# Performance work log

Hardware: AMD Instinct MI355X
Metric: run time of the kernel (lower is better)

## Reference

```python
import jax, jax.numpy as jnp
import numpy as np

L, B, T, D, H, F = 6, 4, 1024, 512, 8, 2048
DH = D // H
BIAS_DIM = 2
E = 65536
EPS = 1e-3  # LayerNormalization default epsilon in the source


def _ln(x, scale, bias):
    m = jnp.mean(x, axis=-1, keepdims=True)
    v = jnp.mean(jnp.square(x - m), axis=-1, keepdims=True)  # tf.nn.moments: population variance
    return (x - m) * jax.lax.rsqrt(v + EPS) * scale + bias


def setup_inputs() -> dict:
    key = jax.random.key(0)
    ks = jax.random.split(key, 24)
    g = lambda k, shape: (jax.random.normal(k, shape, jnp.float32) * (shape[-1] ** -0.5))
    states = jax.random.normal(ks[0], (B, T, D), jnp.float32)
    # causal mask broadcast over heads: [B, 1, Tq, Tk]
    masks = jnp.tril(jnp.ones((T, T), jnp.float32))[None, None] * jnp.ones((B, 1, 1, 1), jnp.float32)
    # sparse bias edges: columns (edge_type, batch_idx, key_idx, query_idx)
    et = jax.random.randint(ks[1], (E, 1), 0, BIAS_DIM)
    bi = jax.random.randint(ks[2], (E, 1), 0, B)
    ki = jax.random.randint(ks[3], (E, 1), 0, T)
    qi = jax.random.randint(ks[4], (E, 1), 0, T)
    attention_bias = jnp.concatenate([et, bi, ki, qi], axis=1).astype(jnp.int32)
    return dict(
        states=states,
        masks=masks,
        attention_bias=attention_bias,
        Wq=g(ks[5], (L, D, H, DH)),
        Wk=g(ks[6], (L, D, H, DH)),
        Wv=g(ks[7], (L, D, H, DH)),
        Wo=g(ks[8], (L, H, DH, D)),
        Eb=g(ks[9], (L, BIAS_DIM, DH)),
        Es=g(ks[10], (L, DH)),
        ln1_s=jnp.ones((L, D), jnp.float32),
        ln1_b=jnp.zeros((L, D), jnp.float32),
        ln2_s=jnp.ones((L, D), jnp.float32),
        ln2_b=jnp.zeros((L, D), jnp.float32),
        lno_s=jnp.ones((D,), jnp.float32),
        lno_b=jnp.zeros((D,), jnp.float32),
        W1=g(ks[11], (L, D, F)),
        b1=jnp.zeros((L, F), jnp.float32),
        W2=g(ks[12], (L, F, D)),
        b2=jnp.zeros((L, D), jnp.float32),
    )


def reference(states, masks, attention_bias, Wq, Wk, Wv, Wo, Eb, Es,
              ln1_s, ln1_b, ln2_s, ln2_b, lno_s, lno_b, W1, b1, W2, b2):
    FMIN = jnp.finfo(jnp.float32).min
    scale = jnp.float32(DH) ** -0.5
    et, bi, ki, qi = (attention_bias[:, 0], attention_bias[:, 1],
                      attention_bias[:, 2], attention_bias[:, 3])
    for l in range(L):
        # --- self-attention with edge bias ---
        x = _ln(states, ln1_s[l], ln1_b[l])
        q = jnp.einsum('btd,dha->btha', x, Wq[l])
        k = jnp.einsum('btd,dha->btha', x, Wk[l])
        v = jnp.einsum('btd,dha->btha', x, Wv[l])
        alpha = jnp.einsum('bkha,bqha->bhqk', k, q)
        # edge-type embedding -> scalar per edge, scatter into dense [B,q,k] (duplicates sum)
        bias_val = Eb[l][et] @ Es[l]  # [E]
        bias3 = jnp.zeros((B, T, T), jnp.float32).at[bi, ki, qi].add(bias_val)
        alpha = alpha + jnp.einsum('bqk,bkh->bhqk', bias3, k.sum(-1))
        alpha = alpha * scale
        alpha = alpha * masks + (1.0 - jnp.ceil(masks)) * FMIN
        alpha = jax.nn.softmax(alpha, axis=-1) * masks  # mask-softmax-renormalize (no renorm, just re-mask)
        ctx = jnp.einsum('bhqk,bkha->bqha', alpha, v)
        states = states + jnp.einsum('btha,had->btd', ctx, Wo[l])
        # --- FFN ---
        h = jax.nn.relu(_ln(states, ln2_s[l], ln2_b[l]) @ W1[l] + b1[l])
        states = states + h @ W2[l] + b2[l]
    return _ln(states, lno_s, lno_b)
```

## Files before the change

kernel.cpp:

```cpp
#include <hip/hip_runtime.h>
#include <hip/hip_bf16.h>
#include <cstdint>

#define LNUM 6
#define BNUM 4
#define TSEQ 1024
#define DMOD 512
#define HNUM 8
#define FDIM 2048
#define DHEAD 64
#define NEVENTS 65536
#define EPS_LN 1e-3f
#define ATT_SCALE 0.125f

#define GF_ACC 1
#define GF_RELU 2
#define GF_BIAS 4
#define GF_SPLIT 8
#define GF_QKV 16
#define GF_PART 32

typedef float f32x4 __attribute__((ext_vector_type(4)));
typedef short bf16x8 __attribute__((ext_vector_type(8)));
typedef unsigned short u16;
typedef unsigned int u32;

__device__ inline u16 f2bf(float f){
  u32 u = __builtin_bit_cast(u32, f);
  u32 r = (u + 0x7fffu + ((u >> 16) & 1u)) >> 16;
  return (u16)r;
}
__device__ inline float bf2f(u16 u){
  return __builtin_bit_cast(float, (u32)u << 16);
}
__device__ inline void split2(float x, u16 &hi, u16 &lo){
  u16 h = f2bf(x);
  lo = f2bf(x - bf2f(h));
  hi = h;
}
__device__ inline void gload16(const void* g, void* l){
  __builtin_amdgcn_global_load_lds(
      (const __attribute__((address_space(1))) void*)g,
      (__attribute__((address_space(3))) void*)l, 16, 0, 0);
}

__global__ __launch_bounds__(256) void ln_kernel(const float* __restrict__ x,
    const float* __restrict__ s, const float* __restrict__ bsh,
    float* __restrict__ yf, u16* __restrict__ yh, u16* __restrict__ yl, int mode){
  int row = blockIdx.x, tid = threadIdx.x;
  const float* xr = x + (size_t)row * DMOD;
  float2 v = *reinterpret_cast<const float2*>(xr + tid*2);
  float sum = v.x + v.y, sq = v.x*v.x + v.y*v.y;
  #pragma unroll
  for (int off = 32; off > 0; off >>= 1){
    sum += __shfl_down(sum, off);
    sq  += __shfl_down(sq, off);
  }
  __shared__ float ss[4], sq2[4];
  int wid = tid >> 6;
  if ((tid & 63) == 0){ ss[wid] = sum; sq2[wid] = sq; }
  __syncthreads();
  sum = ss[0]+ss[1]+ss[2]+ss[3];
  sq  = sq2[0]+sq2[1]+sq2[2]+sq2[3];
  float mean = sum * (1.f/DMOD);
  float var  = sq * (1.f/DMOD) - mean*mean;
  float rstd = rsqrtf(var + EPS_LN);
  float2 sc = *reinterpret_cast<const float2*>(s + tid*2);
  float2 bi = *reinterpret_cast<const float2*>(bsh + tid*2);
  float ox = (v.x - mean)*rstd*sc.x + bi.x;
  float oy = (v.y - mean)*rstd*sc.y + bi.y;
  if (mode == 0){
    u16 h0,l0,h1,l1;
    split2(ox,h0,l0); split2(oy,h1,l1);
    *(u32*)(yh + (size_t)row*DMOD + tid*2) = (u32)h0 | ((u32)h1<<16);
    *(u32*)(yl + (size_t)row*DMOD + tid*2) = (u32)l0 | ((u32)l1<<16);
  } else {
    float2 o; o.x = ox; o.y = oy;
    *reinterpret_cast<float2*>(yf + (size_t)row*DMOD + tid*2) = o;
  }
}

__global__ __launch_bounds__(256) void wsplit5(
    const float* __restrict__ Wq, const float* __restrict__ Wk,
    const float* __restrict__ Wv, const float* __restrict__ Wo,
    const float* __restrict__ W1, int l,
    u16* __restrict__ wqkvh, u16* __restrict__ wqkvl,
    u16* __restrict__ woh,   u16* __restrict__ wol,
    u16* __restrict__ w1h,   u16* __restrict__ w1l){
  __shared__ float T[64][65];
  int id = blockIdx.x;
  const float* src; u16 *dh, *dl; int N, bx, by;
  if (id < 256){
    const int which = id >> 6, sub = id & 63;
    bx = sub & 7; by = sub >> 3; N = 512;
    if (which == 0){ src = Wq; dh = wqkvh;            dl = wqkvl; }
    else if (which == 1){ src = Wk; dh = wqkvh + 512*512; dl = wqkvl + 512*512; }
    else if (which == 2){ src = Wv; dh = wqkvh + 2*512*512; dl = wqkvl + 2*512*512; }
    else { src = Wo; dh = woh; dl = wol; }
    src += (size_t)l*DMOD*DMOD;
  } else {
    id -= 256;
    bx = id & 31; by = id >> 5; N = 2048;
    src = W1 + (size_t)l*DMOD*FDIM; dh = w1h; dl = w1l;
  }
  const int k0 = by*64, n0 = bx*64;
  const int tid = threadIdx.x;
  {
    const int r = tid>>2, cseg = (tid&3)*16;
    const float* sp = src + (size_t)(k0+r)*N + n0 + cseg;
    #pragma unroll
    for (int i = 0; i < 16; i += 4){
      float4 v = *(const float4*)(sp + i);
      T[cseg+i+0][r] = v.x; T[cseg+i+1][r] = v.y;
      T[cseg+i+2][r] = v.z; T[cseg+i+3][r] = v.w;
    }
  }
  __syncthreads();
  const int n = tid>>2, kseg = (tid&3)*16;
  u32 wh[8], wl[8];
  #pragma unroll
  for (int i = 0; i < 8; ++i){
    u16 h0,l0,h1,l1;
    split2(T[n][kseg+2*i], h0, l0);
    split2(T[n][kseg+2*i+1], h1, l1);
    wh[i] = (u32)h0 | ((u32)h1<<16);
    wl[i] = (u32)l0 | ((u32)l1<<16);
  }
  u16* ph = dh + (size_t)(n0+n)*DMOD + k0 + kseg;
  u16* pl = dl + (size_t)(n0+n)*DMOD + k0 + kseg;
  *(uint4*)(ph)   = make_uint4(wh[0],wh[1],wh[2],wh[3]);
  *(uint4*)(ph+8) = make_uint4(wh[4],wh[5],wh[6],wh[7]);
  *(uint4*)(pl)   = make_uint4(wl[0],wl[1],wl[2],wl[3]);
  *(uint4*)(pl+8) = make_uint4(wl[4],wl[5],wl[6],wl[7]);
}

__global__ __launch_bounds__(256) void wsplit(const float* __restrict__ W,
    u16* __restrict__ Thi, u16* __restrict__ Tlo, int K, int N){
  __shared__ float T[64][65];
  const int k0 = blockIdx.y*64, n0 = blockIdx.x*64;
  const int tid = threadIdx.x;
  {
    const int r = tid>>2, cseg = (tid&3)*16;
    const float* src = W + (size_t)(k0+r)*N + n0 + cseg;
    #pragma unroll
    for (int i = 0; i < 16; i += 4){
      float4 v = *(const float4*)(src + i);
      T[cseg+i+0][r] = v.x; T[cseg+i+1][r] = v.y;
      T[cseg+i+2][r] = v.z; T[cseg+i+3][r] = v.w;
    }
  }
  __syncthreads();
  const int n = tid>>2, kseg = (tid&3)*16;
  u32 wh[8], wl[8];
  #pragma unroll
  for (int i = 0; i < 8; ++i){
    u16 h0,l0,h1,l1;
    split2(T[n][kseg+2*i], h0, l0);
    split2(T[n][kseg+2*i+1], h1, l1);
    wh[i] = (u32)h0 | ((u32)h1<<16);
    wl[i] = (u32)l0 | ((u32)l1<<16);
  }
  u16* dh = Thi + (size_t)(n0+n)*K + k0 + kseg;
  u16* dl = Tlo + (size_t)(n0+n)*K + k0 + kseg;
  *(uint4*)(dh)   = make_uint4(wh[0],wh[1],wh[2],wh[3]);
  *(uint4*)(dh+8) = make_uint4(wh[4],wh[5],wh[6],wh[7]);
  *(uint4*)(dl)   = make_uint4(wl[0],wl[1],wl[2],wl[3]);
  *(uint4*)(dl+8) = make_uint4(wl[4],wl[5],wl[6],wl[7]);
}

template<int BN, int NS, int FLAGS>
__global__ __launch_bounds__(256) void gemm_mfma(
    const u16* __restrict__ Ahi, const u16* __restrict__ Alo,
    const u16* __restrict__ Bhi, const u16* __restrict__ Blo,
    const float* __restrict__ bias, float* __restrict__ C,
    u16* __restrict__ Ohi, u16* __restrict__ Olo,
    u16* __restrict__ Vhi, u16* __restrict__ Vlo,
    int M, int N, int K, int kc){
  constexpr int NA  = 16;
  constexpr int NB  = BN/8;
  constexpr int PER = (NA+NB)/4;
  __shared__ __align__(16) unsigned char As[128*128];
  __shared__ __align__(16) unsigned char Bs[BN*128];
  const int tid = threadIdx.x, wid = tid>>6, lane = tid&63;
  const int li = lane&15, g = lane>>4;
  const int nxb = N/BN;
  const int cpx = gridDim.x >> 3;
  const int bid = blockIdx.x;
  const int wg  = (bid&7)*cpx + (bid>>3);
  const int bx = wg % nxb, by = wg / nxb;
  const int m0 = by*128, n0 = bx*BN;
  const int wr = wid>>1, wc = wid&1;
  const int kbeg = blockIdx.y * kc, kend = kbeg + kc;
  f32x4 acc[4][NS] = {};

  for (int k0 = kbeg; k0 < kend; k0 += 32){
    __syncthreads();
    #pragma unroll
    for (int i = 0; i < PER; ++i){
      const int issue = wid*PER + i;
      const bool isA = issue < NA;
      const int ia = isA ? issue : issue - NA;
      const int c = ia*64 + lane;
      const int row = c>>3, slot = c&7;
      const int sg = slot ^ (row&7);
      const u16* base = isA ? (sg < 4 ? Ahi : Alo) : (sg < 4 ? Bhi : Blo);
      const int gr = (isA ? m0 : n0) + row;
      const u16* gp = base + (size_t)gr*K + k0 + (sg&3)*8;
      unsigned char* lp = (isA ? As : Bs) + ia*1024 + lane*16;
      gload16(gp, lp);
    }
    __syncthreads();
    bf16x8 ah[4], al[4], bh[NS], bl[NS];
    #pragma unroll
    for (int ms = 0; ms < 4; ++ms){
      const int r = wr*64 + ms*16 + li; const int x = (r&7)<<4;
      const unsigned char* p = As + r*128;
      ah[ms] = *(const bf16x8*)(p + ((g*16)^x));
      al[ms] = *(const bf16x8*)(p + ((64 + g*16)^x));
    }
    #pragma unroll
    for (int ns = 0; ns < NS; ++ns){
      const int r = wc*(BN/2) + ns*16 + li; const int x = (r&7)<<4;
      const unsigned char* p = Bs + r*128;
      bh[ns] = *(const bf16x8*)(p + ((g*16)^x));
      bl[ns] = *(const bf16x8*)(p + ((64 + g*16)^x));
    }
    #pragma unroll
    for (int ms = 0; ms < 4; ++ms)
      #pragma unroll
      for (int ns = 0; ns < NS; ++ns){
        acc[ms][ns] = __builtin_amdgcn_mfma_f32_16x16x32_bf16(ah[ms], bh[ns], acc[ms][ns], 0, 0, 0);
        acc[ms][ns] = __builtin_amdgcn_mfma_f32_16x16x32_bf16(ah[ms], bl[ns], acc[ms][ns], 0, 0, 0);
        acc[ms][ns] = __builtin_amdgcn_mfma_f32_16x16x32_bf16(al[ms], bh[ns], acc[ms][ns], 0, 0, 0);
      }
  }
  #pragma unroll
  for (int ms = 0; ms < 4; ++ms){
    #pragma unroll
    for (int ns = 0; ns < NS; ++ns){
      #pragma unroll
      for (int r = 0; r < 4; ++r){
        const int m = m0 + wr*64 + ms*16 + g*4 + r;
        const int n = n0 + wc*(BN/2) + ns*16 + li;
        float val = acc[ms][ns][r];
        if (FLAGS & GF_BIAS) val += bias[n];
        if (FLAGS & GF_RELU) val = fmaxf(val, 0.f);
        if (FLAGS & GF_QKV){
          u16 vh, vl; split2(val, vh, vl);
          if (n < 1024){
            const size_t ix = (size_t)m*1024 + n;
            Ohi[ix] = vh; Olo[ix] = vl;
          } else {
            const size_t ix = ((size_t)(m>>10)*DMOD + (n-1024))*TSEQ + (m&1023);
            Vhi[ix] = vh; Vlo[ix] = vl;
          }
        } else if (FLAGS & GF_SPLIT){
          u16 vh, vl; split2(val, vh, vl);
          const size_t ix = (size_t)m*N + n;
          Ohi[ix] = vh; Olo[ix] = vl;
        } else if (FLAGS & GF_PART){
          C[(size_t)blockIdx.y*M*N + (size_t)m*N + n] = val;
        } else {
          const size_t ix = (size_t)m*N + n;
          if (FLAGS & GF_ACC) val += C[ix];
          C[ix] = val;
        }
      }
    }
  }
}

__global__ __launch_bounds__(256) void red2(const float* __restrict__ part,
    const float* __restrict__ bias, float* __restrict__ states, int hasb){
  const size_t MN = (size_t)BNUM*TSEQ*DMOD;
  const size_t i4 = ((size_t)blockIdx.x*256 + threadIdx.x)*4;
  float4 a = *(const float4*)(part + i4);
  float4 b = *(const float4*)(part + MN + i4);
  float4 s = *(const float4*)(states + i4);
  s.x += a.x + b.x;
  s.y += a.y + b.y;
  s.z += a.z + b.z;
  s.w += a.w + b.w;
  if (hasb){
    float4 bb = *(const float4*)(bias + (int)(i4 & (DMOD-1)));
    s.x += bb.x; s.y += bb.y; s.z += bb.z; s.w += bb.w;
  }
  *(float4*)(states + i4) = s;
}

__global__ __launch_bounds__(256) void ksum_kernel(const u16* __restrict__ kh_,
    const u16* __restrict__ kl_, float* __restrict__ ks){
  int idx = blockIdx.x*256 + threadIdx.x;
  const size_t base = (size_t)(idx>>3)*1024 + 512 + (idx&7)*DHEAD;
  const u16* ph = kh_ + base;
  const u16* pl = kl_ + base;
  float s = 0.f;
  #pragma unroll
  for (int a = 0; a < DHEAD; a += 8){
    bf16x8 vh = *(const bf16x8*)(ph + a);
    bf16x8 vl = *(const bf16x8*)(pl + a);
    #pragma unroll
    for (int j = 0; j < 8; ++j) s += bf2f((u16)vh[j]) + bf2f((u16)vl[j]);
  }
  ks[idx] = s;
}

__global__ __launch_bounds__(256) void scatter_kernel(const int* __restrict__ ab,
    const float* __restrict__ Eb, const float* __restrict__ Es, float* __restrict__ bias3){
  __shared__ float d2[2];
  if (threadIdx.x < 2){
    float v = 0.f;
    #pragma unroll
    for (int a = 0; a < DHEAD; ++a) v += Eb[threadIdx.x*DHEAD + a]*Es[a];
    d2[threadIdx.x] = v;
  }
  __syncthreads();
  int e = blockIdx.x*256 + threadIdx.x;
  int4 r = *reinterpret_cast<const int4*>(ab + (size_t)e*4);
  atomicAdd(bias3 + ((size_t)r.y*TSEQ + r.z)*TSEQ + r.w, d2[r.x]);
}

__device__ __forceinline__ void tile_compute(
    const unsigned char* __restrict__ Klh, const unsigned char* __restrict__ Kll,
    const unsigned char* __restrict__ Vh, const unsigned char* __restrict__ Vl,
    unsigned char* __restrict__ Plh, unsigned char* __restrict__ Pll,
    const float* __restrict__ ksl, const float* __restrict__ bb,
    int kt, int rowg0, int wid, int li, int g,
    const bf16x8* qah, const bf16x8* qal,
    f32x4* oacc, float* mrun, float* srun){
  f32x4 sacc[4] = {};
  #pragma unroll
  for (int jb = 0; jb < 4; ++jb){
    const int rb = (jb*16 + li)*128, x = (li & 7) << 4;
    #pragma unroll
    for (int k2 = 0; k2 < 2; ++k2){
      bf16x8 kfh = *(const bf16x8*)(Klh + rb + ((g*16 + k2*64)^x));
      bf16x8 kfl = *(const bf16x8*)(Kll + rb + ((g*16 + k2*64)^x));
      sacc[jb] = __builtin_amdgcn_mfma_f32_16x16x32_bf16(qah[k2], kfh, sacc[jb], 0, 0, 0);
      sacc[jb] = __builtin_amdgcn_mfma_f32_16x16x32_bf16(qah[k2], kfl, sacc[jb], 0, 0, 0);
      sacc[jb] = __builtin_amdgcn_mfma_f32_16x16x32_bf16(qal[k2], kfh, sacc[jb], 0, 0, 0);
    }
  }
  #pragma unroll
  for (int jb = 0; jb < 4; ++jb){
    const int colg = kt + jb*16 + li;
    const float ksv = ksl[jb*16 + li];
    #pragma unroll
    for (int r = 0; r < 4; ++r){
      const int rowg = rowg0 + r;
      float s = (sacc[jb][r] + bb[(size_t)rowg*TSEQ + colg] * ksv) * ATT_SCALE;
      sacc[jb][r] = (colg <= rowg) ? s : -INFINITY;
    }
  }
  #pragma unroll
  for (int r = 0; r < 4; ++r){
    float tm = fmaxf(fmaxf(sacc[0][r], sacc[1][r]), fmaxf(sacc[2][r], sacc[3][r]));
    tm = fmaxf(tm, __shfl_xor(tm, 1));
    tm = fmaxf(tm, __shfl_xor(tm, 2));
    tm = fmaxf(tm, __shfl_xor(tm, 4));
    tm = fmaxf(tm, __shfl_xor(tm, 8));
    const float nm = fmaxf(mrun[r], tm);
    const float fac = __expf(mrun[r] - nm);
    mrun[r] = nm;
    float p0 = __expf(sacc[0][r] - nm);
    float p1 = __expf(sacc[1][r] - nm);
    float p2 = __expf(sacc[2][r] - nm);
    float p3 = __expf(sacc[3][r] - nm);
    float rs = p0 + p1 + p2 + p3;
    rs += __shfl_xor(rs, 1);
    rs += __shfl_xor(rs, 2);
    rs += __shfl_xor(rs, 4);
    rs += __shfl_xor(rs, 8);
    srun[r] = srun[r]*fac + rs;
    oacc[0][r] *= fac; oacc[1][r] *= fac; oacc[2][r] *= fac; oacc[3][r] *= fac;
    const int prow = g*4 + r;
    const int pb = wid*2048 + prow*128, px = (prow & 7) << 4;
    u16 ph0,pl0, ph1,pl1, ph2,pl2, ph3,pl3;
    split2(p0,ph0,pl0); split2(p1,ph1,pl1); split2(p2,ph2,pl2); split2(p3,ph3,pl3);
    *(u16*)(Plh + pb + ((li*2 +  0)^px)) = ph0;
    *(u16*)(Plh + pb + ((li*2 + 32)^px)) = ph1;
    *(u16*)(Plh + pb + ((li*2 + 64)^px)) = ph2;
    *(u16*)(Plh + pb + ((li*2 + 96)^px)) = ph3;
    *(u16*)(Pll + pb + ((li*2 +  0)^px)) = pl0;
    *(u16*)(Pll + pb + ((li*2 + 32)^px)) = pl1;
    *(u16*)(Pll + pb + ((li*2 + 64)^px)) = pl2;
    *(u16*)(Pll + pb + ((li*2 + 96)^px)) = pl3;
  }
  bf16x8 pah[2], pal[2];
  {
    const int pb = wid*2048 + li*128, x = (li & 7) << 4;
    pah[0] = *(const bf16x8*)(Plh + pb + ((g*16     )^x));
    pah[1] = *(const bf16x8*)(Plh + pb + ((g*16 + 64)^x));
    pal[0] = *(const bf16x8*)(Pll + pb + ((g*16     )^x));
    pal[1] = *(const bf16x8*)(Pll + pb + ((g*16 + 64)^x));
  }
  #pragma unroll
  for (int ja = 0; ja < 4; ++ja){
    const int vb = (ja*16 + li)*128, x = (li & 7) << 4;
    #pragma unroll
    for (int k2 = 0; k2 < 2; ++k2){
      bf16x8 vfh = *(const bf16x8*)(Vh + vb + ((g*16 + k2*64)^x));
      bf16x8 vfl = *(const bf16x8*)(Vl + vb + ((g*16 + k2*64)^x));
      oacc[ja] = __builtin_amdgcn_mfma_f32_16x16x32_bf16(pah[k2], vfh, oacc[ja], 0, 0, 0);
      oacc[ja] = __builtin_amdgcn_mfma_f32_16x16x32_bf16(pah[k2], vfl, oacc[ja], 0, 0, 0);
      oacc[ja] = __builtin_amdgcn_mfma_f32_16x16x32_bf16(pal[k2], vfh, oacc[ja], 0, 0, 0);
    }
  }
}

__global__ __launch_bounds__(256) void attn_split(
    const u16* __restrict__ qkh, const u16* __restrict__ qkl,
    const u16* __restrict__ vth, const u16* __restrict__ vtl,
    const float* __restrict__ ksum, const float* __restrict__ bias3,
    u16* __restrict__ ch_, u16* __restrict__ cl_){
  __shared__ __align__(16) unsigned char Klh[8192], Kll[8192], Vh[8192], Vl[8192];
  __shared__ __align__(16) unsigned char Plh[8192], Pll[8192];
  __shared__ float ksl[64];

  const int bid = blockIdx.x;
  const int p = bid & 7, h = (bid >> 3) & 7, b = bid >> 6;
  const int qA0 = p*64, qB0 = (15-p)*64;
  const int tid = threadIdx.x, wid = tid >> 6, lane = tid & 63;
  const int li = lane & 15, g = lane >> 4;
  const int rowA0 = qA0 + wid*16 + g*4;
  const int rowB0 = qB0 + wid*16 + g*4;

  bf16x8 qahA[2], qalA[2], qahB[2], qalB[2];
  {
    const size_t offA = (size_t)(b*TSEQ + qA0 + wid*16 + li)*1024 + h*DHEAD;
    const size_t offB = (size_t)(b*TSEQ + qB0 + wid*16 + li)*1024 + h*DHEAD;
    #pragma unroll
    for (int k2 = 0; k2 < 2; ++k2){
      qahA[k2] = *(const bf16x8*)(qkh + offA + g*8 + k2*32);
      qalA[k2] = *(const bf16x8*)(qkl + offA + g*8 + k2*32);
      qahB[k2] = *(const bf16x8*)(qkh + offB + g*8 + k2*32);
      qalB[k2] = *(const bf16x8*)(qkl + offB + g*8 + k2*32);
    }
  }

  f32x4 oaccA[4] = {}, oaccB[4] = {};
  float mrunA[4] = {-INFINITY,-INFINITY,-INFINITY,-INFINITY};
  float mrunB[4] = {-INFINITY,-INFINITY,-INFINITY,-INFINITY};
  float srunA[4] = {0.f,0.f,0.f,0.f};
  float srunB[4] = {0.f,0.f,0.f,0.f};

  const int krow = tid >> 2, part = tid & 3;
  const int lbase = krow*128, lx = (krow & 7) << 4;
  const float* bb = bias3 + (size_t)b*TSEQ*TSEQ;

  uint4 rk0, rk1, rk2, rk3, rv0, rv1, rv2, rv3;
  float ksr = 0.f;
  auto issue = [&](int kt){
    const size_t koff = (size_t)(b*TSEQ + kt + krow)*1024 + 512 + h*DHEAD + part*16;
    rk0 = *(const uint4*)(qkh + koff);
    rk1 = *(const uint4*)(qkh + koff + 8);
    rk2 = *(const uint4*)(qkl + koff);
    rk3 = *(const uint4*)(qkl + koff + 8);
    const size_t voff = ((size_t)b*DMOD + h*DHEAD + krow)*TSEQ + kt + part*16;
    rv0 = *(const uint4*)(vth + voff);
    rv1 = *(const uint4*)(vth + voff + 8);
    rv2 = *(const uint4*)(vtl + voff);
    rv3 = *(const uint4*)(vtl + voff + 8);
    if (tid < 64) ksr = ksum[(size_t)(b*TSEQ + kt + tid)*HNUM + h];
  };

  issue(0);
  for (int kt = 0; kt <= qB0; kt += 64){
    *(uint4*)(Klh + lbase + ((part*32     )^lx)) = rk0;
    *(uint4*)(Klh + lbase + ((part*32 + 16)^lx)) = rk1;
    *(uint4*)(Kll + lbase + ((part*32     )^lx)) = rk2;
    *(uint4*)(Kll + lbase + ((part*32 + 16)^lx)) = rk3;
    *(uint4*)(Vh  + lbase + ((part*32     )^lx)) = rv0;
    *(uint4*)(Vh  + lbase + ((part*32 + 16)^lx)) = rv1;
    *(uint4*)(Vl  + lbase + ((part*32     )^lx)) = rv2;
    *(uint4*)(Vl  + lbase + ((part*32 + 16)^lx)) = rv3;
    if (tid < 64) ksl[tid] = ksr;
    __syncthreads();
    if (kt + 64 <= qB0) issue(kt + 64);
    tile_compute(Klh, Kll, Vh, Vl, Plh, Pll, ksl, bb, kt, rowB0, wid, li, g,
                 qahB, qalB, oaccB, mrunB, srunB);
    if (kt <= qA0)
      tile_compute(Klh, Kll, Vh, Vl, Plh, Pll, ksl, bb, kt, rowA0, wid, li, g,
                   qahA, qalA, oaccA, mrunA, srunA);
    __syncthreads();
  }

  #pragma unroll
  for (int ja = 0; ja < 4; ++ja){
    #pragma unroll
    for (int r = 0; r < 4; ++r){
      {
        const float val = oaccB[ja][r] / srunB[r];
        u16 vh, vl; split2(val, vh, vl);
        const size_t ix = (size_t)(b*TSEQ + rowB0 + r)*DMOD + h*DHEAD + ja*16 + li;
        ch_[ix] = vh; cl_[ix] = vl;
      }
      {
        const float val = oaccA[ja][r] / srunA[r];
        u16 vh, vl; split2(val, vh, vl);
        const size_t ix = (size_t)(b*TSEQ + rowA0 + r)*DMOD + h*DHEAD + ja*16 + li;
        ch_[ix] = vh; cl_[ix] = vl;
      }
    }
  }
}

extern "C" void kernel_launch(void* const* d_in, const int* in_sizes, int n_in,
                              void* d_out, int out_size, void* d_ws, size_t ws_size,
                              hipStream_t stream){
  const float* states0 = (const float*)d_in[0];
  const int*   ab      = (const int*)d_in[2];
  const float* Wq = (const float*)d_in[3];
  const float* Wk = (const float*)d_in[4];
  const float* Wv = (const float*)d_in[5];
  const float* Wo = (const float*)d_in[6];
  const float* Eb = (const float*)d_in[7];
  const float* Es = (const float*)d_in[8];
  const float* ln1_s = (const float*)d_in[9];
  const float* ln1_b = (const float*)d_in[10];
  const float* ln2_s = (const float*)d_in[11];
  const float* ln2_b = (const float*)d_in[12];
  const float* lno_s = (const float*)d_in[13];
  const float* lno_b = (const float*)d_in[14];
  const float* W1 = (const float*)d_in[15];
  const float* b1 = (const float*)d_in[16];
  const float* W2 = (const float*)d_in[17];
  const float* b2 = (const float*)d_in[18];
  float* out = (float*)d_out;

  char* ws = (char*)d_ws;
  const size_t MB = 1024*1024;
  float* states = (float*)(ws);
  u16* xh  = (u16*)(ws + 8*MB);
  u16* xl  = (u16*)(ws + 12*MB);
  u16* qkh = (u16*)(ws + 16*MB);
  u16* qkl = (u16*)(ws + 24*MB);
  u16* vth = (u16*)(ws + 32*MB);
  u16* vtl = (u16*)(ws + 36*MB);
  u16* cth = (u16*)(ws + 40*MB);
  u16* ctl = (u16*)(ws + 44*MB);
  float* ksum  = (float*)(ws + 48*MB);
  float* bias3 = (float*)(ws + 48*MB + 131072);
  char*  wA    = ws + 64*MB + 131072;
  char*  wB    = wA + 4*MB;
  u16* hh = qkh;
  u16* hl = vth;
  float* part = bias3;

  u16* wqkvh = (u16*)(wA);
  u16* wqkvl = (u16*)(wA + 1536*1024);
  u16* woh   = (u16*)(wA + 3*MB);
  u16* wol   = (u16*)(wA + 3*MB + 512*1024);
  u16* w2h   = (u16*)(wA);
  u16* w2l   = (u16*)(wA + 2*MB);
  u16* w1h   = (u16*)(wB);
  u16* w1l   = (u16*)(wB + 2*MB);

  hipMemcpyAsync(states, states0, 8*MB, hipMemcpyDeviceToDevice, stream);

  const int NROW = BNUM*TSEQ;
  dim3 blk(256);
  for (int l = 0; l < LNUM; ++l){
    wsplit5<<<512, blk, 0, stream>>>(Wq, Wk, Wv, Wo, W1, l,
        wqkvh, wqkvl, woh, wol, w1h, w1l);

    ln_kernel<<<NROW, blk, 0, stream>>>(states, ln1_s + l*DMOD, ln1_b + l*DMOD, nullptr, xh, xl, 0);
    gemm_mfma<128,4, GF_SPLIT|GF_QKV><<<384, blk, 0, stream>>>(
        xh, xl, wqkvh, wqkvl, nullptr, nullptr, qkh, qkl, vth, vtl, NROW, 1536, DMOD, DMOD);
    ksum_kernel<<<(BNUM*TSEQ*HNUM)/256, blk, 0, stream>>>(qkh, qkl, ksum);
    hipMemsetAsync(bias3, 0, (size_t)BNUM*TSEQ*TSEQ*sizeof(float), stream);
    scatter_kernel<<<NEVENTS/256, blk, 0, stream>>>(ab, Eb + (size_t)l*2*DHEAD, Es + (size_t)l*DHEAD, bias3);
    attn_split<<<BNUM*HNUM*8, blk, 0, stream>>>(qkh, qkl, vth, vtl, ksum, bias3, cth, ctl);
    gemm_mfma<64,2, GF_PART><<<dim3(256,2), blk, 0, stream>>>(
        cth, ctl, woh, wol, nullptr, part, nullptr, nullptr, nullptr, nullptr, NROW, DMOD, DMOD, DMOD/2);
    red2<<<(NROW*DMOD)/1024, blk, 0, stream>>>(part, b2, states, 0);

    wsplit<<<dim3(8,32), blk, 0, stream>>>(W2 + (size_t)l*FDIM*DMOD, w2h, w2l, FDIM, DMOD);
    ln_kernel<<<NROW, blk, 0, stream>>>(states, ln2_s + l*DMOD, ln2_b + l*DMOD, nullptr, xh, xl, 0);
    gemm_mfma<128,4, GF_BIAS|GF_RELU|GF_SPLIT><<<512, blk, 0, stream>>>(
        xh, xl, w1h, w1l, b1 + (size_t)l*FDIM, nullptr, hh, hl, nullptr, nullptr, NROW, FDIM, DMOD, DMOD);
    gemm_mfma<64,2, GF_PART><<<dim3(256,2), blk, 0, stream>>>(
        hh, hl, w2h, w2l, nullptr, part, nullptr, nullptr, nullptr, nullptr, NROW, DMOD, FDIM, FDIM/2);
    red2<<<(NROW*DMOD)/1024, blk, 0, stream>>>(part, b2 + (size_t)l*DMOD, states, 1);
  }
  ln_kernel<<<NROW, blk, 0, stream>>>(states, lno_s, lno_b, out, nullptr, nullptr, 1);
}
```

Baseline: 1.314 ms.

## Fuse split-K reduction into layernorm and split attention KV loop across two groups

The red2 reduction kernels are removed. Summing the two split-K partials plus the FFN bias into the residual now happens inside the following layernorm kernel, which writes the updated states back. Attention blocks grow to 512 threads: two 256-thread groups process alternating key tiles with separate LDS buffers, then merge their online-softmax states (max, sum, output) through shared memory. This cuts one launch and one full read/write pass per residual add, and doubles per-block parallelism over the key loop, at the cost of about 97KB of LDS per block and an extra merge step.

```diff
diff --git a/kernel.cpp b/kernel.cpp
--- a/kernel.cpp
+++ b/kernel.cpp
@@ -44,12 +44,24 @@
       (__attribute__((address_space(3))) void*)l, 16, 0, 0);
 }
 
-__global__ __launch_bounds__(256) void ln_kernel(const float* __restrict__ x,
+__global__ __launch_bounds__(256) void ln_kernel(float* __restrict__ x,
+    const float* __restrict__ part, const float* __restrict__ abias,
     const float* __restrict__ s, const float* __restrict__ bsh,
     float* __restrict__ yf, u16* __restrict__ yh, u16* __restrict__ yl, int mode){
   int row = blockIdx.x, tid = threadIdx.x;
-  const float* xr = x + (size_t)row * DMOD;
+  float* xr = x + (size_t)row * DMOD;
   float2 v = *reinterpret_cast<const float2*>(xr + tid*2);
+  if (part){
+    const size_t MN = (size_t)BNUM*TSEQ*DMOD;
+    const size_t o = (size_t)row*DMOD + tid*2;
+    float2 p0 = *reinterpret_cast<const float2*>(part + o);
+    float2 p1 = *reinterpret_cast<const float2*>(part + MN + o);
+    v.x += p0.x + p1.x; v.y += p0.y + p1.y;
+    if (abias){
+      v.x += abias[tid*2]; v.y += abias[tid*2+1];
+    }
+    *reinterpret_cast<float2*>(xr + tid*2) = v;
+  }
   float sum = v.x + v.y, sq = v.x*v.x + v.y*v.y;
   #pragma unroll
   for (int off = 32; off > 0; off >>= 1){
@@ -268,24 +280,6 @@
       }
     }
   }
-}
-
-__global__ __launch_bounds__(256) void red2(const float* __restrict__ part,
-    const float* __restrict__ bias, float* __restrict__ states, int hasb){
-  const size_t MN = (size_t)BNUM*TSEQ*DMOD;
-  const size_t i4 = ((size_t)blockIdx.x*256 + threadIdx.x)*4;
-  float4 a = *(const float4*)(part + i4);
-  float4 b = *(const float4*)(part + MN + i4);
-  float4 s = *(const float4*)(states + i4);
-  s.x += a.x + b.x;
-  s.y += a.y + b.y;
-  s.z += a.z + b.z;
-  s.w += a.w + b.w;
-  if (hasb){
-    float4 bb = *(const float4*)(bias + (int)(i4 & (DMOD-1)));
-    s.x += bb.x; s.y += bb.y; s.z += bb.z; s.w += bb.w;
-  }
-  *(float4*)(states + i4) = s;
 }
 
 __global__ __launch_bounds__(256) void ksum_kernel(const u16* __restrict__ kh_,
@@ -408,27 +402,39 @@
   }
 }
 
-__global__ __launch_bounds__(256) void attn_split(
+__global__ __launch_bounds__(512) void attn_split(
     const u16* __restrict__ qkh, const u16* __restrict__ qkl,
     const u16* __restrict__ vth, const u16* __restrict__ vtl,
     const float* __restrict__ ksum, const float* __restrict__ bias3,
     u16* __restrict__ ch_, u16* __restrict__ cl_){
-  __shared__ __align__(16) unsigned char Klh[8192], Kll[8192], Vh[8192], Vl[8192];
-  __shared__ __align__(16) unsigned char Plh[8192], Pll[8192];
-  __shared__ float ksl[64];
+  __shared__ __align__(16) unsigned char smem[99328];
+  unsigned char* PlhAll = smem + 65536;
+  unsigned char* PllAll = smem + 81920;
+  float* kslAll = (float*)(smem + 98304);
 
   const int bid = blockIdx.x;
   const int p = bid & 7, h = (bid >> 3) & 7, b = bid >> 6;
   const int qA0 = p*64, qB0 = (15-p)*64;
-  const int tid = threadIdx.x, wid = tid >> 6, lane = tid & 63;
-  const int li = lane & 15, g = lane >> 4;
-  const int rowA0 = qA0 + wid*16 + g*4;
-  const int rowB0 = qB0 + wid*16 + g*4;
+  const int tid = threadIdx.x;
+  const int grp = tid >> 8, t = tid & 255;
+  const int wid = tid >> 6;
+  const int wid4 = t >> 6;
+  const int lane = tid & 63, li = lane & 15, g = lane >> 4;
+  const int rowA0 = qA0 + wid4*16 + g*4;
+  const int rowB0 = qB0 + wid4*16 + g*4;
+  const int NB = 16 - p, NA = p + 1;
+  const int ITER = (NB + 1) >> 1;
+
+  unsigned char* Klh = smem + grp*32768;
+  unsigned char* Kll = Klh + 8192;
+  unsigned char* Vh  = Klh + 16384;
+  unsigned char* Vl  = Klh + 24576;
+  float* kslg = kslAll + grp*64;
 
   bf16x8 qahA[2], qalA[2], qahB[2], qalB[2];
   {
-    const size_t offA = (size_t)(b*TSEQ + qA0 + wid*16 + li)*1024 + h*DHEAD;
-    const size_t offB = (size_t)(b*TSEQ + qB0 + wid*16 + li)*1024 + h*DHEAD;
+    const size_t offA = (size_t)(b*TSEQ + qA0 + wid4*16 + li)*1024 + h*DHEAD;
+    const size_t offB = (size_t)(b*TSEQ + qB0 + wid4*16 + li)*1024 + h*DHEAD;
     #pragma unroll
     for (int k2 = 0; k2 < 2; ++k2){
       qahA[k2] = *(const bf16x8*)(qkh + offA + g*8 + k2*32);
@@ -444,7 +450,7 @@
   float srunA[4] = {0.f,0.f,0.f,0.f};
   float srunB[4] = {0.f,0.f,0.f,0.f};
 
-  const int krow = tid >> 2, part = tid & 3;
+  const int krow = t >> 2, part = t & 3;
   const int lbase = krow*128, lx = (krow & 7) << 4;
   const float* bb = bias3 + (size_t)b*TSEQ*TSEQ;
 
@@ -461,45 +467,90 @@
     rv1 = *(const uint4*)(vth + voff + 8);
     rv2 = *(const uint4*)(vtl + voff);
     rv3 = *(const uint4*)(vtl + voff + 8);
-    if (tid < 64) ksr = ksum[(size_t)(b*TSEQ + kt + tid)*HNUM + h];
+    if (t < 64) ksr = ksum[(size_t)(b*TSEQ + kt + t)*HNUM + h];
   };
 
-  issue(0);
-  for (int kt = 0; kt <= qB0; kt += 64){
-    *(uint4*)(Klh + lbase + ((part*32     )^lx)) = rk0;
-    *(uint4*)(Klh + lbase + ((part*32 + 16)^lx)) = rk1;
-    *(uint4*)(Kll + lbase + ((part*32     )^lx)) = rk2;
-    *(uint4*)(Kll + lbase + ((part*32 + 16)^lx)) = rk3;
-    *(uint4*)(Vh  + lbase + ((part*32     )^lx)) = rv0;
-    *(uint4*)(Vh  + lbase + ((part*32 + 16)^lx)) = rv1;
-    *(uint4*)(Vl  + lbase + ((part*32     )^lx)) = rv2;
-    *(uint4*)(Vl  + lbase + ((part*32 + 16)^lx)) = rv3;
-    if (tid < 64) ksl[tid] = ksr;
+  issue(grp*64);
+  for (int it = 0; it < ITER; ++it){
+    const int idx = it*2 + grp;
+    const bool act = idx < NB;
+    if (act){
+      *(uint4*)(Klh + lbase + ((part*32     )^lx)) = rk0;
+      *(uint4*)(Klh + lbase + ((part*32 + 16)^lx)) = rk1;
+      *(uint4*)(Kll + lbase + ((part*32     )^lx)) = rk2;
+      *(uint4*)(Kll + lbase + ((part*32 + 16)^lx)) = rk3;
+      *(uint4*)(Vh  + lbase + ((part*32     )^lx)) = rv0;
+      *(uint4*)(Vh  + lbase + ((part*32 + 16)^lx)) = rv1;
+      *(uint4*)(Vl  + lbase + ((part*32     )^lx)) = rv2;
+      *(uint4*)(Vl  + lbase + ((part*32 + 16)^lx)) = rv3;
+      if (t < 64) kslg[t] = ksr;
+    }
     __syncthreads();
-    if (kt + 64 <= qB0) issue(kt + 64);
-    tile_compute(Klh, Kll, Vh, Vl, Plh, Pll, ksl, bb, kt, rowB0, wid, li, g,
-                 qahB, qalB, oaccB, mrunB, srunB);
-    if (kt <= qA0)
-      tile_compute(Klh, Kll, Vh, Vl, Plh, Pll, ksl, bb, kt, rowA0, wid, li, g,
-                   qahA, qalA, oaccA, mrunA, srunA);
+    if (idx + 2 < NB) issue((idx + 2)*64);
+    if (act){
+      const int kt = idx*64;
+      tile_compute(Klh, Kll, Vh, Vl, PlhAll, PllAll, kslg, bb, kt, rowB0,
+                   wid, li, g, qahB, qalB, oaccB, mrunB, srunB);
+      if (idx < NA)
+        tile_compute(Klh, Kll, Vh, Vl, PlhAll, PllAll, kslg, bb, kt, rowA0,
+                     wid, li, g, qahA, qalA, oaccA, mrunA, srunA);
+    }
     __syncthreads();
   }
 
-  #pragma unroll
-  for (int ja = 0; ja < 4; ++ja){
+  float* MO = (float*)smem;
+  float* MS = (float*)(smem + 32768);
+  if (grp == 1){
     #pragma unroll
     for (int r = 0; r < 4; ++r){
+      const int rr = wid4*16 + g*4 + r;
+      #pragma unroll
+      for (int ja = 0; ja < 4; ++ja){
+        MO[(0*64 + rr)*64 + ja*16 + li] = oaccB[ja][r];
+        MO[(1*64 + rr)*64 + ja*16 + li] = oaccA[ja][r];
+      }
+      if (li == 0){
+        MS[(0*64 + rr)*2 + 0] = mrunB[r];
+        MS[(0*64 + rr)*2 + 1] = srunB[r];
+        MS[(1*64 + rr)*2 + 0] = mrunA[r];
+        MS[(1*64 + rr)*2 + 1] = srunA[r];
+      }
+    }
+  }
+  __syncthreads();
+  if (grp == 0){
+    #pragma unroll
+    for (int r = 0; r < 4; ++r){
+      const int rr = wid4*16 + g*4 + r;
       {
-        const float val = oaccB[ja][r] / srunB[r];
-        u16 vh, vl; split2(val, vh, vl);
-        const size_t ix = (size_t)(b*TSEQ + rowB0 + r)*DMOD + h*DHEAD + ja*16 + li;
-        ch_[ix] = vh; cl_[ix] = vl;
+        const float m1 = MS[(0*64+rr)*2+0], s1 = MS[(0*64+rr)*2+1];
+        const float m = fmaxf(mrunB[r], m1);
+        const float f0 = __expf(mrunB[r] - m);
+        const float f1 = (s1 > 0.f) ? __expf(m1 - m) : 0.f;
+        const float sinv = 1.f / (srunB[r]*f0 + s1*f1);
+        #pragma unroll
+        for (int ja = 0; ja < 4; ++ja){
+          const float o1 = MO[(0*64+rr)*64 + ja*16 + li];
+          const float val = (oaccB[ja][r]*f0 + o1*f1) * sinv;
+          u16 vh, vl; split2(val, vh, vl);
+          const size_t ix = (size_t)(b*TSEQ + qB0 + rr)*DMOD + h*DHEAD + ja*16 + li;
+          ch_[ix] = vh; cl_[ix] = vl;
+        }
       }
       {
-        const float val = oaccA[ja][r] / srunA[r];
-        u16 vh, vl; split2(val, vh, vl);
-        const size_t ix = (size_t)(b*TSEQ + rowA0 + r)*DMOD + h*DHEAD + ja*16 + li;
-        ch_[ix] = vh; cl_[ix] = vl;
+        const float m1 = MS[(1*64+rr)*2+0], s1 = MS[(1*64+rr)*2+1];
+        const float m = fmaxf(mrunA[r], m1);
+        const float f0 = __expf(mrunA[r] - m);
+        const float f1 = (s1 > 0.f) ? __expf(m1 - m) : 0.f;
+        const float sinv = 1.f / (srunA[r]*f0 + s1*f1);
+        #pragma unroll
+        for (int ja = 0; ja < 4; ++ja){
+          const float o1 = MO[(1*64+rr)*64 + ja*16 + li];
+          const float val = (oaccA[ja][r]*f0 + o1*f1) * sinv;
+          u16 vh, vl; split2(val, vh, vl);
+          const size_t ix = (size_t)(b*TSEQ + qA0 + rr)*DMOD + h*DHEAD + ja*16 + li;
+          ch_[ix] = vh; cl_[ix] = vl;
+        }
       }
     }
   }
@@ -564,24 +615,26 @@
     wsplit5<<<512, blk, 0, stream>>>(Wq, Wk, Wv, Wo, W1, l,
         wqkvh, wqkvl, woh, wol, w1h, w1l);
 
-    ln_kernel<<<NROW, blk, 0, stream>>>(states, ln1_s + l*DMOD, ln1_b + l*DMOD, nullptr, xh, xl, 0);
+    ln_kernel<<<NROW, blk, 0, stream>>>(states,
+        (l == 0) ? nullptr : part, (l == 0) ? nullptr : b2 + (size_t)(l-1)*DMOD,
+        ln1_s + l*DMOD, ln1_b + l*DMOD, nullptr, xh, xl, 0);
     gemm_mfma<128,4, GF_SPLIT|GF_QKV><<<384, blk, 0, stream>>>(
         xh, xl, wqkvh, wqkvl, nullptr, nullptr, qkh, qkl, vth, vtl, NROW, 1536, DMOD, DMOD);
     ksum_kernel<<<(BNUM*TSEQ*HNUM)/256, blk, 0, stream>>>(qkh, qkl, ksum);
     hipMemsetAsync(bias3, 0, (size_t)BNUM*TSEQ*TSEQ*sizeof(float), stream);
     scatter_kernel<<<NEVENTS/256, blk, 0, stream>>>(ab, Eb + (size_t)l*2*DHEAD, Es + (size_t)l*DHEAD, bias3);
-    attn_split<<<BNUM*HNUM*8, blk, 0, stream>>>(qkh, qkl, vth, vtl, ksum, bias3, cth, ctl);
+    attn_split<<<BNUM*HNUM*8, dim3(512), 0, stream>>>(qkh, qkl, vth, vtl, ksum, bias3, cth, ctl);
     gemm_mfma<64,2, GF_PART><<<dim3(256,2), blk, 0, stream>>>(
         cth, ctl, woh, wol, nullptr, part, nullptr, nullptr, nullptr, nullptr, NROW, DMOD, DMOD, DMOD/2);
-    red2<<<(NROW*DMOD)/1024, blk, 0, stream>>>(part, b2, states, 0);
 
     wsplit<<<dim3(8,32), blk, 0, stream>>>(W2 + (size_t)l*FDIM*DMOD, w2h, w2l, FDIM, DMOD);
-    ln_kernel<<<NROW, blk, 0, stream>>>(states, ln2_s + l*DMOD, ln2_b + l*DMOD, nullptr, xh, xl, 0);
+    ln_kernel<<<NROW, blk, 0, stream>>>(states, part, nullptr,
+        ln2_s + l*DMOD, ln2_b + l*DMOD, nullptr, xh, xl, 0);
     gemm_mfma<128,4, GF_BIAS|GF_RELU|GF_SPLIT><<<512, blk, 0, stream>>>(
         xh, xl, w1h, w1l, b1 + (size_t)l*FDIM, nullptr, hh, hl, nullptr, nullptr, NROW, FDIM, DMOD, DMOD);
     gemm_mfma<64,2, GF_PART><<<dim3(256,2), blk, 0, stream>>>(
         hh, hl, w2h, w2l, nullptr, part, nullptr, nullptr, nullptr, nullptr, NROW, DMOD, FDIM, FDIM/2);
-    red2<<<(NROW*DMOD)/1024, blk, 0, stream>>>(part, b2 + (size_t)l*DMOD, states, 1);
-  }
-  ln_kernel<<<NROW, blk, 0, stream>>>(states, lno_s, lno_b, out, nullptr, nullptr, 1);
-}
+  }
+  ln_kernel<<<NROW, blk, 0, stream>>>(states, part, b2 + (size_t)(LNUM-1)*DMOD,
+      lno_s, lno_b, out, nullptr, nullptr, 1);
+}
```

Result: slower. 1.516 ms (+15.4%).
